# Kernel optimization log

Hardware: AMD Instinct MI355X
Metric: run time of the kernel (lower is better)

## Reference

```python
import jax, jax.numpy as jnp
import numpy as np

B, S, D, H = 2, 2048, 1024, 16
DK = D // H


def setup_inputs() -> dict:
    key = jax.random.key(0)
    ks = jax.random.split(key, 8)
    q = jax.random.normal(ks[0], (B, S, D), dtype=jnp.float32)
    k = jax.random.normal(ks[1], (B, S, D), dtype=jnp.float32)
    v = jax.random.normal(ks[2], (B, S, D), dtype=jnp.float32)
    mask = jax.random.randint(ks[3], (B, 1, S, S), 0, 2, dtype=jnp.int32)
    sc = 1.0 / np.sqrt(D)
    Wq = jax.random.normal(ks[4], (D, D), dtype=jnp.float32) * sc
    Wk = jax.random.normal(ks[5], (D, D), dtype=jnp.float32) * sc
    Wv = jax.random.normal(ks[6], (D, D), dtype=jnp.float32) * sc
    Wo = jax.random.normal(ks[7], (D, D), dtype=jnp.float32) * sc
    return {"q": q, "k": k, "v": v, "mask": mask, "Wq": Wq, "Wk": Wk, "Wv": Wv, "Wo": Wo}


def reference(q, k, v, mask, Wq, Wk, Wv, Wo):
    # Linear projections (torch Linear: x @ W.T; bias=False). Weights here stored
    # as [D, D] applied as x @ W (equivalent parameterization).
    query = q @ Wq  # [B,S,D]
    key = k @ Wk
    value = v @ Wv
    # split heads -> [B,H,S,DK]
    query = query.reshape(B, S, H, DK).transpose(0, 2, 1, 3)
    key = key.reshape(B, S, H, DK).transpose(0, 2, 1, 3)
    value = value.reshape(B, S, H, DK).transpose(0, 2, 1, 3)
    scores = jnp.einsum('bhqd,bhkd->bhqk', query, key) / jnp.sqrt(jnp.float32(DK))
    scores = jnp.where(mask == 0, jnp.float32(-1e9), scores)
    probs = jax.nn.softmax(scores, axis=-1)  # dropout p=0.0 -> identity
    x = jnp.einsum('bhqk,bhkd->bhqd', probs, value)
    x = x.transpose(0, 2, 1, 3).reshape(B, S, D)
    return x @ Wo
```

## Files before the change

### kernel.cpp

```cpp
#include <hip/hip_runtime.h>
#include <hip/hip_bf16.h>

#define B_ 2
#define S_ 2048
#define D_ 1024
#define H_ 16
#define DK_ 64
#define SW_ (S_ / 64)

typedef unsigned short u16;
typedef unsigned int u32;
typedef unsigned long long u64;
typedef __attribute__((ext_vector_type(8))) short short8;
typedef __attribute__((ext_vector_type(4))) float float4_;
typedef __attribute__((ext_vector_type(4))) unsigned int uint4_;

static __device__ inline u16 f_to_bf16(float f) {
    union { float f; u32 i; } x; x.f = f;
    u32 r = x.i + 0x7fff + ((x.i >> 16) & 1);
    return (u16)(r >> 16);
}

static __device__ __forceinline__ u32 pack2(float a, float b) {
    union { float f; u32 i; } xa, xb; xa.f = a; xb.f = b;
    return ((xa.i + 0x8000u) >> 16) | ((xb.i + 0x8000u) & 0xffff0000u);
}

static __device__ inline void gl_lds16(const u16* g, u16* l) {
    __builtin_amdgcn_global_load_lds((const __attribute__((address_space(1))) void*)g,
                                     (__attribute__((address_space(3))) void*)l, 16, 0, 0);
}

__global__ __launch_bounds__(256) void mpack(const int* __restrict__ mask,
                                             u64* __restrict__ mp) {
    int wv = (blockIdx.x * 256 + threadIdx.x) >> 6;
    int lane = threadIdx.x & 63;
    #pragma unroll
    for (int i = 0; i < 8; ++i) {
        int wd = wv * 8 + i;
        u64 bits = __ballot(mask[(size_t)wd * 64 + lane] != 0);
        if (lane == 0) mp[wd] = bits;
    }
}

__global__ __launch_bounds__(256) void cvt3(const float* __restrict__ q,
                                            const float* __restrict__ k,
                                            const float* __restrict__ v,
                                            u16* __restrict__ qb,
                                            u16* __restrict__ kb,
                                            u16* __restrict__ vb, int n) {
    int z = blockIdx.z;
    const float* s = (z == 0) ? q : ((z == 1) ? k : v);
    u16* d = (z == 0) ? qb : ((z == 1) ? kb : vb);
    int i = (blockIdx.x * 256 + threadIdx.x) * 8;
    if (i >= n) return;
    #pragma unroll
    for (int j = 0; j < 8; ++j) d[i + j] = f_to_bf16(s[i + j]);
}

__global__ __launch_bounds__(256) void wtrans4(const float* __restrict__ W0,
                                               const float* __restrict__ W1,
                                               const float* __restrict__ W2,
                                               const float* __restrict__ W3,
                                               u16* __restrict__ T0, u16* __restrict__ T1,
                                               u16* __restrict__ T2, u16* __restrict__ T3) {
    __shared__ float tile[32][33];
    int z = blockIdx.z;
    const float* W = (z == 0) ? W0 : ((z == 1) ? W1 : ((z == 2) ? W2 : W3));
    u16* Wt = (z == 0) ? T0 : ((z == 1) ? T1 : ((z == 2) ? T2 : T3));
    int k0 = blockIdx.x * 32, n0 = blockIdx.y * 32;
    int tx = threadIdx.x & 31, ty = threadIdx.x >> 5;
    #pragma unroll
    for (int i = 0; i < 4; ++i) {
        int row = ty + i * 8;
        tile[row][tx] = W[(size_t)(k0 + row) * D_ + n0 + tx];
    }
    __syncthreads();
    #pragma unroll
    for (int i = 0; i < 4; ++i) {
        int row = ty + i * 8;
        Wt[(size_t)(n0 + row) * D_ + k0 + tx] = f_to_bf16(tile[tx][row]);
    }
}

static __device__ __forceinline__ void gemm128_body(u16* lds,
                                                    const u16* __restrict__ A,
                                                    const u16* __restrict__ Bt,
                                                    int K, float4_ (&acc)[4][4]) {
    u16* ldsA = lds;
    u16* ldsB = lds + 4096;
    int tm = blockIdx.x, tn = blockIdx.y;
    int t = threadIdx.x, l = t & 63;
    int w = t >> 6, wr = w >> 1, wc = w & 1;
    int colL = l & 15, grp = l >> 4;
    int sw4 = (grp ^ ((colL >> 1) & 3)) << 3;
    int f0 = t, f1 = t + 256;
    int row0 = f0 >> 2, kc0 = (((f0 & 3) ^ ((f0 >> 3) & 3)) << 3);
    int row1 = f1 >> 2, kc1 = (((f1 & 3) ^ ((f1 >> 3) & 3)) << 3);
    const u16* gA0 = A  + (size_t)(tm * 128 + row0) * K + kc0;
    const u16* gA1 = A  + (size_t)(tm * 128 + row1) * K + kc1;
    const u16* gB0 = Bt + (size_t)(tn * 128 + row0) * K + kc0;
    const u16* gB1 = Bt + (size_t)(tn * 128 + row1) * K + kc1;

    #pragma unroll
    for (int mi = 0; mi < 4; ++mi)
        #pragma unroll
        for (int ni = 0; ni < 4; ++ni)
            acc[mi][ni] = (float4_){0.f, 0.f, 0.f, 0.f};

    for (int k0 = 0; k0 < K; k0 += 32) {
        __syncthreads();
        gl_lds16(gA0 + k0, ldsA + f0 * 8);
        gl_lds16(gA1 + k0, ldsA + f1 * 8);
        gl_lds16(gB0 + k0, ldsB + f0 * 8);
        gl_lds16(gB1 + k0, ldsB + f1 * 8);
        __syncthreads();
        short8 a[4], b[4];
        #pragma unroll
        for (int mi = 0; mi < 4; ++mi)
            a[mi] = *(const short8*)&ldsA[(wr * 64 + mi * 16 + colL) * 32 + sw4];
        #pragma unroll
        for (int ni = 0; ni < 4; ++ni)
            b[ni] = *(const short8*)&ldsB[(wc * 64 + ni * 16 + colL) * 32 + sw4];
        #pragma unroll
        for (int mi = 0; mi < 4; ++mi)
            #pragma unroll
            for (int ni = 0; ni < 4; ++ni)
                acc[mi][ni] = __builtin_amdgcn_mfma_f32_16x16x32_bf16(a[mi], b[ni], acc[mi][ni], 0, 0, 0);
    }
}

__global__ __launch_bounds__(256) void gemm_qkv(const u16* __restrict__ qb,
                                                const u16* __restrict__ kb,
                                                const u16* __restrict__ vb,
                                                const u16* __restrict__ Wqt,
                                                const u16* __restrict__ Wkt,
                                                const u16* __restrict__ Wvt,
                                                u16* __restrict__ Qp,
                                                u16* __restrict__ Kp,
                                                u16* __restrict__ Vt) {
    __shared__ u16 lds[8192];
    int z = blockIdx.z;
    const u16* A  = (z == 0) ? qb  : ((z == 1) ? kb  : vb);
    const u16* Bt = (z == 0) ? Wqt : ((z == 1) ? Wkt : Wvt);
    float4_ acc[4][4];
    gemm128_body(lds, A, Bt, D_, acc);

    int tm = blockIdx.x, tn = blockIdx.y;
    int t = threadIdx.x, l = t & 63;
    int w = t >> 6, wr = w >> 1, wc = w & 1;
    int colL = l & 15, grp = l >> 4;

    if (z < 2) {
        u16* Y = (z == 0) ? Qp : Kp;
        float sc = (z == 0) ? 0.125f : 1.0f;
        #pragma unroll
        for (int mi = 0; mi < 4; ++mi)
            #pragma unroll
            for (int ni = 0; ni < 4; ++ni)
                #pragma unroll
                for (int r = 0; r < 4; ++r)
                    Y[(size_t)(tm * 128 + wr * 64 + mi * 16 + grp * 4 + r) * D_
                      + tn * 128 + wc * 64 + ni * 16 + colL] = f_to_bf16(acc[mi][ni][r] * sc);
    } else {
        __syncthreads();
        int bglob = tm >> 4;
        int hh = tn * 2 + wc;
        u16* vt_out = Vt + (size_t)(bglob * H_ + hh) * DK_ * S_;
        #pragma unroll
        for (int rnd = 0; rnd < 2; ++rnd) {
            if (wr == rnd) {
                u16* tb = lds + wc * 4096;
                #pragma unroll
                for (int mi = 0; mi < 4; ++mi)
                    #pragma unroll
                    for (int r = 0; r < 4; ++r) {
                        int m = mi * 16 + grp * 4 + r;
                        int mp_ = (m >> 5) * 32 + ((m >> 2) & 3) * 8 + ((m >> 4) & 1) * 4 + (m & 3);
                        #pragma unroll
                        for (int ni = 0; ni < 4; ++ni) {
                            int nl = ni * 16 + colL;
                            tb[nl * 64 + (mp_ ^ ((nl & 7) << 3))] = f_to_bf16(acc[mi][ni][r]);
                        }
                    }
                int s_base = (tm & 15) * 128 + rnd * 64;
                #pragma unroll
                for (int p = 0; p < 8; ++p) {
                    int row = p * 8 + (l >> 3);
                    int ch = l & 7;
                    short8 val = *(const short8*)&tb[row * 64 + ((ch ^ (row & 7)) << 3)];
                    *(short8*)&vt_out[(size_t)row * S_ + s_base + ch * 8] = val;
                }
            }
            __syncthreads();
        }
    }
}

__global__ __launch_bounds__(256) void gemm_out(const u16* __restrict__ Xa,
                                                const u16* __restrict__ Wot,
                                                float* __restrict__ out) {
    __shared__ u16 lds[8192];
    float4_ acc[4][4];
    gemm128_body(lds, Xa, Wot, D_, acc);

    int tm = blockIdx.x, tn = blockIdx.y;
    int t = threadIdx.x, l = t & 63;
    int w = t >> 6, wr = w >> 1, wc = w & 1;
    int colL = l & 15, grp = l >> 4;
    #pragma unroll
    for (int mi = 0; mi < 4; ++mi)
        #pragma unroll
        for (int ni = 0; ni < 4; ++ni)
            #pragma unroll
            for (int r = 0; r < 4; ++r)
                out[(size_t)(tm * 128 + wr * 64 + mi * 16 + grp * 4 + r) * D_
                    + tn * 128 + wc * 64 + ni * 16 + colL] = acc[mi][ni][r];
}

__global__ __launch_bounds__(256) void attn64(const u16* __restrict__ Qp,
                                              const u16* __restrict__ Kp,
                                              const u16* __restrict__ Vt,
                                              const u64* __restrict__ mp,
                                              u16* __restrict__ Xa) {
    __shared__ u16 ldsK[64 * 64];
    __shared__ u16 ldsV[64 * 64];

    int bid = blockIdx.x;
    int qt = bid & 31, h = (bid >> 5) & 15, b = bid >> 9;
    int t = threadIdx.x, l = t & 63, w = t >> 6;
    int colL = l & 15, grp = l >> 4;

    const u16* qbase = Qp + (size_t)(b * S_ + qt * 64 + w * 16 + colL) * D_ + h * DK_;
    short8 qf0 = *(const short8*)(qbase + grp * 8);
    short8 qf1 = *(const short8*)(qbase + 32 + grp * 8);

    int f0 = t, f1 = t + 256;
    int kr0 = f0 >> 3, kc0 = (((f0 & 7) ^ (kr0 & 7)) << 3);
    int kr1 = f1 >> 3, kc1 = (((f1 & 7) ^ (kr1 & 7)) << 3);
    const u16* gK0 = Kp + (size_t)(b * S_ + kr0) * D_ + h * DK_ + kc0;
    const u16* gK1 = Kp + (size_t)(b * S_ + kr1) * D_ + h * DK_ + kc1;
    const u16* gVb = Vt + (size_t)(b * H_ + h) * DK_ * S_;
    const u16* gV0 = gVb + (size_t)kr0 * S_ + kc0;
    const u16* gV1 = gVb + (size_t)kr1 * S_ + kc1;

    int sw8 = (grp ^ (colL & 7)) << 3;

    float l_run = 0.f;
    float4_ o[4];
    #pragma unroll
    for (int nt = 0; nt < 4; ++nt) o[nt] = (float4_){0.f, 0.f, 0.f, 0.f};

    const u64* mrow = mp + (size_t)(b * S_ + qt * 64 + w * 16 + colL) * SW_;

    for (int kt = 0; kt < S_; kt += 64) {
        u64 mw = mrow[kt >> 6];

        __syncthreads();
        gl_lds16(gK0 + (size_t)kt * D_, ldsK + f0 * 8);
        gl_lds16(gK1 + (size_t)kt * D_, ldsK + f1 * 8);
        gl_lds16(gV0 + kt,              ldsV + f0 * 8);
        gl_lds16(gV1 + kt,              ldsV + f1 * 8);
        __syncthreads();

        float4_ s[4];
        #pragma unroll
        for (int nt = 0; nt < 4; ++nt) {
            int ro = (nt * 16 + colL) * 64;
            short8 kf0 = *(const short8*)&ldsK[ro + sw8];
            short8 kf1 = *(const short8*)&ldsK[ro + (sw8 ^ 32)];
            s[nt] = (float4_){0.f, 0.f, 0.f, 0.f};
            s[nt] = __builtin_amdgcn_mfma_f32_16x16x32_bf16(kf0, qf0, s[nt], 0, 0, 0);
            s[nt] = __builtin_amdgcn_mfma_f32_16x16x32_bf16(kf1, qf1, s[nt], 0, 0, 0);
        }

        u64 mwsh = mw >> (grp * 4);
        #pragma unroll
        for (int nt = 0; nt < 4; ++nt)
            #pragma unroll
            for (int r = 0; r < 4; ++r) {
                float p = __expf(s[nt][r]);
                p = ((mwsh >> (nt * 16 + r)) & 1ull) ? p : 0.f;
                s[nt][r] = p;
                l_run += p;
            }

        uint4_ A1 = { pack2(s[0][0], s[0][1]), pack2(s[0][2], s[0][3]),
                      pack2(s[1][0], s[1][1]), pack2(s[1][2], s[1][3]) };
        uint4_ A2 = { pack2(s[2][0], s[2][1]), pack2(s[2][2], s[2][3]),
                      pack2(s[3][0], s[3][1]), pack2(s[3][2], s[3][3]) };
        short8 pf1 = __builtin_bit_cast(short8, A1);
        short8 pf2 = __builtin_bit_cast(short8, A2);

        #pragma unroll
        for (int nt = 0; nt < 4; ++nt) {
            int ro = (nt * 16 + colL) * 64;
            short8 vf0 = *(const short8*)&ldsV[ro + sw8];
            short8 vf1 = *(const short8*)&ldsV[ro + (sw8 ^ 32)];
            o[nt] = __builtin_amdgcn_mfma_f32_16x16x32_bf16(pf1, vf0, o[nt], 0, 0, 0);
            o[nt] = __builtin_amdgcn_mfma_f32_16x16x32_bf16(pf2, vf1, o[nt], 0, 0, 0);
        }
    }

    l_run += __shfl_xor(l_run, 16, 64);
    l_run += __shfl_xor(l_run, 32, 64);
    float inv[4];
    #pragma unroll
    for (int r = 0; r < 4; ++r)
        inv[r] = 1.f / __shfl(l_run, grp * 4 + r, 64);

    u16* xo = Xa + (size_t)(b * S_ + qt * 64 + w * 16 + grp * 4) * D_ + h * DK_;
    #pragma unroll
    for (int r = 0; r < 4; ++r)
        #pragma unroll
        for (int nt = 0; nt < 4; ++nt)
            xo[(size_t)r * D_ + nt * 16 + colL] = f_to_bf16(o[nt][r] * inv[r]);
}

extern "C" void kernel_launch(void* const* d_in, const int* in_sizes, int n_in,
                              void* d_out, int out_size, void* d_ws, size_t ws_size,
                              hipStream_t stream) {
    const float* q    = (const float*)d_in[0];
    const float* k    = (const float*)d_in[1];
    const float* v    = (const float*)d_in[2];
    const int*   mask = (const int*)d_in[3];
    const float* Wq   = (const float*)d_in[4];
    const float* Wk   = (const float*)d_in[5];
    const float* Wv   = (const float*)d_in[6];
    const float* Wo   = (const float*)d_in[7];
    float* out = (float*)d_out;

    const int NQ = B_ * S_ * D_;
    const int NW = D_ * D_;
    const int NMW = B_ * S_ * SW_;

    u16* qb  = (u16*)d_ws;
    u16* kb  = qb  + NQ;
    u16* vb  = kb  + NQ;
    u16* Wqt = vb  + NQ;
    u16* Wkt = Wqt + NW;
    u16* Wvt = Wkt + NW;
    u16* Wot = Wvt + NW;
    u16* Qp  = Wot + NW;
    u16* Kp  = Qp  + NQ;
    u16* Vt  = Kp  + NQ;
    u16* Xa  = Vt  + NQ;
    u64* mpk = (u64*)(Xa + NQ);

    dim3 cblk(256);
    mpack<<<NMW / (8 * 4), cblk, 0, stream>>>(mask, mpk);
    cvt3<<<dim3(NQ / 2048, 1, 3), cblk, 0, stream>>>(q, k, v, qb, kb, vb, NQ);
    wtrans4<<<dim3(D_ / 32, D_ / 32, 4), cblk, 0, stream>>>(Wq, Wk, Wv, Wo, Wqt, Wkt, Wvt, Wot);

    const int M = B_ * S_;
    gemm_qkv<<<dim3(M / 128, D_ / 128, 3), cblk, 0, stream>>>(qb, kb, vb, Wqt, Wkt, Wvt, Qp, Kp, Vt);

    attn64<<<B_ * H_ * (S_ / 64), cblk, 0, stream>>>(Qp, Kp, Vt, mpk, Xa);

    gemm_out<<<dim3(M / 128, D_ / 128), cblk, 0, stream>>>(Xa, Wot, out);
}
```

Baseline: 293.1 us.

## Fuse prep kernels, widen attention key tile, use exp2, simplify V store

Merges the mask-pack, input-convert and weight-transpose kernels into one launch, which removes two kernel launches. The attention kernel now processes 128 keys per iteration instead of 64, halving the number of barrier pairs, and uses exp2f with log2(e) folded into the Q scale. The V-transpose epilogue drops its LDS staging and barriers and writes scattered 2-byte stores straight to global memory. Occupancy hints are added to the launch bounds. The scattered V stores and larger register footprint could offset some of the gains.

After: 266.1 us. 1.1x faster.

```diff
diff --git a/kernel.cpp b/kernel.cpp
--- a/kernel.cpp
+++ b/kernel.cpp
@@ -1,5 +1,6 @@
 #include <hip/hip_runtime.h>
 #include <hip/hip_bf16.h>
+#include <math.h>
 
 #define B_ 2
 #define S_ 2048
@@ -31,55 +32,58 @@
                                      (__attribute__((address_space(3))) void*)l, 16, 0, 0);
 }
 
-__global__ __launch_bounds__(256) void mpack(const int* __restrict__ mask,
-                                             u64* __restrict__ mp) {
-    int wv = (blockIdx.x * 256 + threadIdx.x) >> 6;
-    int lane = threadIdx.x & 63;
-    #pragma unroll
-    for (int i = 0; i < 8; ++i) {
-        int wd = wv * 8 + i;
-        u64 bits = __ballot(mask[(size_t)wd * 64 + lane] != 0);
-        if (lane == 0) mp[wd] = bits;
-    }
-}
-
-__global__ __launch_bounds__(256) void cvt3(const float* __restrict__ q,
+__global__ __launch_bounds__(256) void prep(const float* __restrict__ q,
                                             const float* __restrict__ k,
                                             const float* __restrict__ v,
-                                            u16* __restrict__ qb,
-                                            u16* __restrict__ kb,
-                                            u16* __restrict__ vb, int n) {
-    int z = blockIdx.z;
-    const float* s = (z == 0) ? q : ((z == 1) ? k : v);
-    u16* d = (z == 0) ? qb : ((z == 1) ? kb : vb);
-    int i = (blockIdx.x * 256 + threadIdx.x) * 8;
-    if (i >= n) return;
-    #pragma unroll
-    for (int j = 0; j < 8; ++j) d[i + j] = f_to_bf16(s[i + j]);
-}
-
-__global__ __launch_bounds__(256) void wtrans4(const float* __restrict__ W0,
-                                               const float* __restrict__ W1,
-                                               const float* __restrict__ W2,
-                                               const float* __restrict__ W3,
-                                               u16* __restrict__ T0, u16* __restrict__ T1,
-                                               u16* __restrict__ T2, u16* __restrict__ T3) {
+                                            const int* __restrict__ mask,
+                                            const float* __restrict__ W0,
+                                            const float* __restrict__ W1,
+                                            const float* __restrict__ W2,
+                                            const float* __restrict__ W3,
+                                            u16* __restrict__ qb, u16* __restrict__ kb,
+                                            u16* __restrict__ vb,
+                                            u16* __restrict__ T0, u16* __restrict__ T1,
+                                            u16* __restrict__ T2, u16* __restrict__ T3,
+                                            u64* __restrict__ mpk) {
     __shared__ float tile[32][33];
-    int z = blockIdx.z;
-    const float* W = (z == 0) ? W0 : ((z == 1) ? W1 : ((z == 2) ? W2 : W3));
-    u16* Wt = (z == 0) ? T0 : ((z == 1) ? T1 : ((z == 2) ? T2 : T3));
-    int k0 = blockIdx.x * 32, n0 = blockIdx.y * 32;
-    int tx = threadIdx.x & 31, ty = threadIdx.x >> 5;
-    #pragma unroll
-    for (int i = 0; i < 4; ++i) {
-        int row = ty + i * 8;
-        tile[row][tx] = W[(size_t)(k0 + row) * D_ + n0 + tx];
-    }
-    __syncthreads();
-    #pragma unroll
-    for (int i = 0; i < 4; ++i) {
-        int row = ty + i * 8;
-        Wt[(size_t)(n0 + row) * D_ + k0 + tx] = f_to_bf16(tile[tx][row]);
+    int gx = blockIdx.x, tid = threadIdx.x;
+    if (gx < 6144) {
+        int z = gx >> 11;
+        int bx = gx & 2047;
+        const float* s = (z == 0) ? q : ((z == 1) ? k : v);
+        u16* d = (z == 0) ? qb : ((z == 1) ? kb : vb);
+        int i = (bx * 256 + tid) * 8;
+        #pragma unroll
+        for (int j = 0; j < 8; ++j) d[i + j] = f_to_bf16(s[i + j]);
+    } else if (gx < 10240) {
+        int g2 = gx - 6144;
+        int z = g2 >> 10;
+        int rem = g2 & 1023;
+        const float* W = (z == 0) ? W0 : ((z == 1) ? W1 : ((z == 2) ? W2 : W3));
+        u16* Wt = (z == 0) ? T0 : ((z == 1) ? T1 : ((z == 2) ? T2 : T3));
+        int k0 = (rem >> 5) * 32, n0 = (rem & 31) * 32;
+        int tx = tid & 31, ty = tid >> 5;
+        #pragma unroll
+        for (int i2 = 0; i2 < 4; ++i2) {
+            int row = ty + i2 * 8;
+            tile[row][tx] = W[(size_t)(k0 + row) * D_ + n0 + tx];
+        }
+        __syncthreads();
+        #pragma unroll
+        for (int i2 = 0; i2 < 4; ++i2) {
+            int row = ty + i2 * 8;
+            Wt[(size_t)(n0 + row) * D_ + k0 + tx] = f_to_bf16(tile[tx][row]);
+        }
+    } else {
+        int g3 = gx - 10240;
+        int wv = (g3 * 256 + tid) >> 6;
+        int lane = tid & 63;
+        #pragma unroll
+        for (int i2 = 0; i2 < 8; ++i2) {
+            int wd = wv * 8 + i2;
+            u64 bits = __ballot(mask[(size_t)wd * 64 + lane] != 0);
+            if (lane == 0) mpk[wd] = bits;
+        }
     }
 }
 
@@ -130,15 +134,15 @@
     }
 }
 
-__global__ __launch_bounds__(256) void gemm_qkv(const u16* __restrict__ qb,
-                                                const u16* __restrict__ kb,
-                                                const u16* __restrict__ vb,
-                                                const u16* __restrict__ Wqt,
-                                                const u16* __restrict__ Wkt,
-                                                const u16* __restrict__ Wvt,
-                                                u16* __restrict__ Qp,
-                                                u16* __restrict__ Kp,
-                                                u16* __restrict__ Vt) {
+__global__ __launch_bounds__(256, 3) void gemm_qkv(const u16* __restrict__ qb,
+                                                   const u16* __restrict__ kb,
+                                                   const u16* __restrict__ vb,
+                                                   const u16* __restrict__ Wqt,
+                                                   const u16* __restrict__ Wkt,
+                                                   const u16* __restrict__ Wvt,
+                                                   u16* __restrict__ Qp,
+                                                   u16* __restrict__ Kp,
+                                                   u16* __restrict__ Vt) {
     __shared__ u16 lds[8192];
     int z = blockIdx.z;
     const u16* A  = (z == 0) ? qb  : ((z == 1) ? kb  : vb);
@@ -153,7 +157,7 @@
 
     if (z < 2) {
         u16* Y = (z == 0) ? Qp : Kp;
-        float sc = (z == 0) ? 0.125f : 1.0f;
+        float sc = (z == 0) ? (0.125f * 1.44269504f) : 1.0f;
         #pragma unroll
         for (int mi = 0; mi < 4; ++mi)
             #pragma unroll
@@ -163,43 +167,29 @@
                     Y[(size_t)(tm * 128 + wr * 64 + mi * 16 + grp * 4 + r) * D_
                       + tn * 128 + wc * 64 + ni * 16 + colL] = f_to_bf16(acc[mi][ni][r] * sc);
     } else {
-        __syncthreads();
-        int bglob = tm >> 4;
-        int hh = tn * 2 + wc;
-        u16* vt_out = Vt + (size_t)(bglob * H_ + hh) * DK_ * S_;
-        #pragma unroll
-        for (int rnd = 0; rnd < 2; ++rnd) {
-            if (wr == rnd) {
-                u16* tb = lds + wc * 4096;
+        int tok_base = tm * 128 + wr * 64;
+        int bb = tok_base >> 11;
+        int s_hi = tok_base & (S_ - 1);
+        #pragma unroll
+        for (int mi = 0; mi < 4; ++mi)
+            #pragma unroll
+            for (int ni = 0; ni < 4; ++ni) {
+                int n  = tn * 128 + wc * 64 + ni * 16 + colL;
+                int hh = n >> 6, dk = n & 63;
+                u16* vp = Vt + ((size_t)(bb * H_ + hh) * DK_ + dk) * S_ + s_hi;
                 #pragma unroll
-                for (int mi = 0; mi < 4; ++mi)
-                    #pragma unroll
-                    for (int r = 0; r < 4; ++r) {
-                        int m = mi * 16 + grp * 4 + r;
-                        int mp_ = (m >> 5) * 32 + ((m >> 2) & 3) * 8 + ((m >> 4) & 1) * 4 + (m & 3);
-                        #pragma unroll
-                        for (int ni = 0; ni < 4; ++ni) {
-                            int nl = ni * 16 + colL;
-                            tb[nl * 64 + (mp_ ^ ((nl & 7) << 3))] = f_to_bf16(acc[mi][ni][r]);
-                        }
-                    }
-                int s_base = (tm & 15) * 128 + rnd * 64;
-                #pragma unroll
-                for (int p = 0; p < 8; ++p) {
-                    int row = p * 8 + (l >> 3);
-                    int ch = l & 7;
-                    short8 val = *(const short8*)&tb[row * 64 + ((ch ^ (row & 7)) << 3)];
-                    *(short8*)&vt_out[(size_t)row * S_ + s_base + ch * 8] = val;
+                for (int r = 0; r < 4; ++r) {
+                    int m = mi * 16 + grp * 4 + r;
+                    int mp_ = ((m >> 5) & 1) * 32 + ((m >> 2) & 3) * 8 + ((m >> 4) & 1) * 4 + (m & 3);
+                    vp[mp_] = f_to_bf16(acc[mi][ni][r]);
                 }
             }
-            __syncthreads();
-        }
-    }
-}
-
-__global__ __launch_bounds__(256) void gemm_out(const u16* __restrict__ Xa,
-                                                const u16* __restrict__ Wot,
-                                                float* __restrict__ out) {
+    }
+}
+
+__global__ __launch_bounds__(256, 3) void gemm_out(const u16* __restrict__ Xa,
+                                                   const u16* __restrict__ Wot,
+                                                   float* __restrict__ out) {
     __shared__ u16 lds[8192];
     float4_ acc[4][4];
     gemm128_body(lds, Xa, Wot, D_, acc);
@@ -218,13 +208,13 @@
                     + tn * 128 + wc * 64 + ni * 16 + colL] = acc[mi][ni][r];
 }
 
-__global__ __launch_bounds__(256) void attn64(const u16* __restrict__ Qp,
-                                              const u16* __restrict__ Kp,
-                                              const u16* __restrict__ Vt,
-                                              const u64* __restrict__ mp,
-                                              u16* __restrict__ Xa) {
-    __shared__ u16 ldsK[64 * 64];
-    __shared__ u16 ldsV[64 * 64];
+__global__ __launch_bounds__(256, 4) void attn128(const u16* __restrict__ Qp,
+                                                  const u16* __restrict__ Kp,
+                                                  const u16* __restrict__ Vt,
+                                                  const u64* __restrict__ mp,
+                                                  u16* __restrict__ Xa) {
+    __shared__ u16 ldsK[128 * 64];
+    __shared__ u16 ldsV[2 * 64 * 64];
 
     int bid = blockIdx.x;
     int qt = bid & 31, h = (bid >> 5) & 15, b = bid >> 9;
@@ -235,14 +225,17 @@
     short8 qf0 = *(const short8*)(qbase + grp * 8);
     short8 qf1 = *(const short8*)(qbase + 32 + grp * 8);
 
-    int f0 = t, f1 = t + 256;
-    int kr0 = f0 >> 3, kc0 = (((f0 & 7) ^ (kr0 & 7)) << 3);
-    int kr1 = f1 >> 3, kc1 = (((f1 & 7) ^ (kr1 & 7)) << 3);
-    const u16* gK0 = Kp + (size_t)(b * S_ + kr0) * D_ + h * DK_ + kc0;
-    const u16* gK1 = Kp + (size_t)(b * S_ + kr1) * D_ + h * DK_ + kc1;
-    const u16* gVb = Vt + (size_t)(b * H_ + h) * DK_ * S_;
-    const u16* gV0 = gVb + (size_t)kr0 * S_ + kc0;
-    const u16* gV1 = gVb + (size_t)kr1 * S_ + kc1;
+    const u16* gK[4];
+    const u16* gV[4];
+    #pragma unroll
+    for (int i = 0; i < 4; ++i) {
+        int f = t + 256 * i;
+        int krow = f >> 3, kch = (((f & 7) ^ (krow & 7)) << 3);
+        gK[i] = Kp + (size_t)(b * S_ + krow) * D_ + h * DK_ + kch;
+        int hreg = f >> 9, fp = f & 511;
+        int vrow = fp >> 3, vch = (((fp & 7) ^ (vrow & 7)) << 3);
+        gV[i] = Vt + ((size_t)(b * H_ + h) * DK_ + vrow) * S_ + hreg * 64 + vch;
+    }
 
     int sw8 = (grp ^ (colL & 7)) << 3;
 
@@ -253,19 +246,22 @@
 
     const u64* mrow = mp + (size_t)(b * S_ + qt * 64 + w * 16 + colL) * SW_;
 
-    for (int kt = 0; kt < S_; kt += 64) {
-        u64 mw = mrow[kt >> 6];
-
-        __syncthreads();
-        gl_lds16(gK0 + (size_t)kt * D_, ldsK + f0 * 8);
-        gl_lds16(gK1 + (size_t)kt * D_, ldsK + f1 * 8);
-        gl_lds16(gV0 + kt,              ldsV + f0 * 8);
-        gl_lds16(gV1 + kt,              ldsV + f1 * 8);
-        __syncthreads();
-
-        float4_ s[4];
-        #pragma unroll
-        for (int nt = 0; nt < 4; ++nt) {
+    for (int kt = 0; kt < S_; kt += 128) {
+        u64 mw0 = mrow[(kt >> 6)];
+        u64 mw1 = mrow[(kt >> 6) + 1];
+
+        __syncthreads();
+        #pragma unroll
+        for (int i = 0; i < 4; ++i) {
+            int f = t + 256 * i;
+            gl_lds16(gK[i] + (size_t)kt * D_, ldsK + f * 8);
+            gl_lds16(gV[i] + kt,              ldsV + f * 8);
+        }
+        __syncthreads();
+
+        float4_ s[8];
+        #pragma unroll
+        for (int nt = 0; nt < 8; ++nt) {
             int ro = (nt * 16 + colL) * 64;
             short8 kf0 = *(const short8*)&ldsK[ro + sw8];
             short8 kf1 = *(const short8*)&ldsK[ro + (sw8 ^ 32)];
@@ -274,31 +270,38 @@
             s[nt] = __builtin_amdgcn_mfma_f32_16x16x32_bf16(kf1, qf1, s[nt], 0, 0, 0);
         }
 
-        u64 mwsh = mw >> (grp * 4);
-        #pragma unroll
-        for (int nt = 0; nt < 4; ++nt)
+        u64 msh0 = mw0 >> (grp * 4), msh1 = mw1 >> (grp * 4);
+        #pragma unroll
+        for (int nt = 0; nt < 8; ++nt) {
+            u64 msh = (nt < 4) ? msh0 : msh1;
             #pragma unroll
             for (int r = 0; r < 4; ++r) {
-                float p = __expf(s[nt][r]);
-                p = ((mwsh >> (nt * 16 + r)) & 1ull) ? p : 0.f;
+                float p = exp2f(s[nt][r]);
+                p = ((msh >> ((nt & 3) * 16 + r)) & 1ull) ? p : 0.f;
                 s[nt][r] = p;
                 l_run += p;
             }
-
-        uint4_ A1 = { pack2(s[0][0], s[0][1]), pack2(s[0][2], s[0][3]),
-                      pack2(s[1][0], s[1][1]), pack2(s[1][2], s[1][3]) };
-        uint4_ A2 = { pack2(s[2][0], s[2][1]), pack2(s[2][2], s[2][3]),
-                      pack2(s[3][0], s[3][1]), pack2(s[3][2], s[3][3]) };
-        short8 pf1 = __builtin_bit_cast(short8, A1);
-        short8 pf2 = __builtin_bit_cast(short8, A2);
+        }
+
+        short8 pf[4];
+        #pragma unroll
+        for (int j = 0; j < 4; ++j) {
+            uint4_ Ax = { pack2(s[2 * j][0], s[2 * j][1]), pack2(s[2 * j][2], s[2 * j][3]),
+                          pack2(s[2 * j + 1][0], s[2 * j + 1][1]), pack2(s[2 * j + 1][2], s[2 * j + 1][3]) };
+            pf[j] = __builtin_bit_cast(short8, Ax);
+        }
 
         #pragma unroll
         for (int nt = 0; nt < 4; ++nt) {
             int ro = (nt * 16 + colL) * 64;
             short8 vf0 = *(const short8*)&ldsV[ro + sw8];
             short8 vf1 = *(const short8*)&ldsV[ro + (sw8 ^ 32)];
-            o[nt] = __builtin_amdgcn_mfma_f32_16x16x32_bf16(pf1, vf0, o[nt], 0, 0, 0);
-            o[nt] = __builtin_amdgcn_mfma_f32_16x16x32_bf16(pf2, vf1, o[nt], 0, 0, 0);
+            short8 vf2 = *(const short8*)&ldsV[4096 + ro + sw8];
+            short8 vf3 = *(const short8*)&ldsV[4096 + ro + (sw8 ^ 32)];
+            o[nt] = __builtin_amdgcn_mfma_f32_16x16x32_bf16(pf[0], vf0, o[nt], 0, 0, 0);
+            o[nt] = __builtin_amdgcn_mfma_f32_16x16x32_bf16(pf[1], vf1, o[nt], 0, 0, 0);
+            o[nt] = __builtin_amdgcn_mfma_f32_16x16x32_bf16(pf[2], vf2, o[nt], 0, 0, 0);
+            o[nt] = __builtin_amdgcn_mfma_f32_16x16x32_bf16(pf[3], vf3, o[nt], 0, 0, 0);
         }
     }
 
@@ -332,7 +335,6 @@
 
     const int NQ = B_ * S_ * D_;
     const int NW = D_ * D_;
-    const int NMW = B_ * S_ * SW_;
 
     u16* qb  = (u16*)d_ws;
     u16* kb  = qb  + NQ;
@@ -348,14 +350,13 @@
     u64* mpk = (u64*)(Xa + NQ);
 
     dim3 cblk(256);
-    mpack<<<NMW / (8 * 4), cblk, 0, stream>>>(mask, mpk);
-    cvt3<<<dim3(NQ / 2048, 1, 3), cblk, 0, stream>>>(q, k, v, qb, kb, vb, NQ);
-    wtrans4<<<dim3(D_ / 32, D_ / 32, 4), cblk, 0, stream>>>(Wq, Wk, Wv, Wo, Wqt, Wkt, Wvt, Wot);
+    prep<<<14336, cblk, 0, stream>>>(q, k, v, mask, Wq, Wk, Wv, Wo,
+                                     qb, kb, vb, Wqt, Wkt, Wvt, Wot, mpk);
 
     const int M = B_ * S_;
     gemm_qkv<<<dim3(M / 128, D_ / 128, 3), cblk, 0, stream>>>(qb, kb, vb, Wqt, Wkt, Wvt, Qp, Kp, Vt);
 
-    attn64<<<B_ * H_ * (S_ / 64), cblk, 0, stream>>>(Qp, Kp, Vt, mpk, Xa);
+    attn128<<<B_ * H_ * (S_ / 64), cblk, 0, stream>>>(Qp, Kp, Vt, mpk, Xa);
 
     gemm_out<<<dim3(M / 128, D_ / 128), cblk, 0, stream>>>(Xa, Wot, out);
 }
```
